# Optimization experiments

Measured on AMD Instinct MI355X. Metric: run time of the kernel, lower is better.

## Reference

```python
import jax, jax.numpy as jnp
import numpy as np

LOG_STD_MAX = 2.0
LOG_STD_MIN = -5.0
HEIGHT = 4          # tree height -> 16 leaves, 15 internal nodes
TOP_K = 4           # top-k leaves kept in soft gate
SMAX_TEMP = 1.0     # softmax temperature over selected leaf logits


def _path_matrix(height: int) -> np.ndarray:
    """[N_internal, L] matrix with +1 where a leaf's root-to-leaf path goes
    left through a node, -1 where it goes right, 0 otherwise."""
    L = 2 ** height
    P = np.zeros((L - 1, L), dtype=np.float32)
    for leaf in range(L):
        node = 0
        for lvl in range(height):
            bit = (leaf >> (height - 1 - lvl)) & 1
            P[node, leaf] = 1.0 if bit == 0 else -1.0
            node = 2 * node + 1 + bit
    return P


def setup_inputs() -> dict:
    key = jax.random.key(0)
    k0, k1, k2, k3, k4 = jax.random.split(key, 5)
    B, D, A = 262144, 128, 8
    L = 2 ** HEIGHT
    N = L - 1
    x = jax.random.normal(k0, (B, D), dtype=jnp.float32)
    Wn = jax.random.normal(k1, (D, N), dtype=jnp.float32) / np.float32(np.sqrt(D))
    bn = jax.random.normal(k2, (N,), dtype=jnp.float32) * 0.01
    Wl = jax.random.normal(k3, (L, D, 2 * A), dtype=jnp.float32) / np.float32(np.sqrt(D))
    bl = jax.random.normal(k4, (L, 2 * A), dtype=jnp.float32) * 0.01
    return {"x": x, "Wn": Wn, "bn": bn, "Wl": Wl, "bl": bl}


def reference(x, Wn, bn, Wl, bl):
    L = Wl.shape[0]
    P = jnp.asarray(_path_matrix(HEIGHT))              # [N, L] constant

    # --- differentiable-tree routing ---
    node_logits = x @ Wn + bn                          # [B, N]
    leaf_logits = node_logits @ P                      # [B, L]
    vals, idx = jax.lax.top_k(leaf_logits, TOP_K)      # [B, k]
    soft = jax.nn.softmax(vals / SMAX_TEMP, axis=-1)   # [B, k]
    onehot = jax.nn.one_hot(idx, L, dtype=x.dtype)     # [B, k, L]
    gate_soft = jnp.einsum('bk,bkl->bl', soft, onehot) # scatter soft weights
    gate_hard = onehot[:, 0]                           # argmax leaf one-hot
    # hard argmax forward, top-k softmax gradient (straight-through)
    gate = gate_hard + gate_soft - jax.lax.stop_gradient(gate_soft)

    # --- per-leaf linear controllers, gated sum ---
    leaf_out = jnp.einsum('bd,ldo->blo', x, Wl) + bl   # [B, L, 2A]
    out = jnp.einsum('bl,blo->bo', gate, leaf_out)     # [B, 2A]

    A = out.shape[-1] // 2
    mean, log_std = out[:, :A], out[:, A:]
    log_std = jnp.tanh(log_std)
    log_std = LOG_STD_MIN + 0.5 * (LOG_STD_MAX - LOG_STD_MIN) * (log_std + 1.0)
    return mean, log_std
```

## Files before the change

kernel.cpp:

```cpp
#include <hip/hip_runtime.h>
#include <math.h>

#define BLK  256
#define DD   128
#define NN   15
#define NL   16
#define OC   16
#define OSTR 20
#define MAXT 32
#define TPW  8
#define GAPTHR 1e-3f

typedef __attribute__((ext_vector_type(8))) short short8v;
typedef __attribute__((ext_vector_type(4))) float f32x4;
typedef union { unsigned u[4]; short8v s; } fragu;

__device__ inline unsigned bf16_rne_u(float f) {
    unsigned u = __float_as_uint(f);
    return (u + 0x7FFFu + ((u >> 16) & 1u)) >> 16;
}
__device__ inline unsigned cvt_pk_bf16(float a, float b) {
    unsigned r;
    asm volatile("v_cvt_pk_bf16_f32 %0, %1, %2" : "=v"(r) : "v"(a), "v"(b));
    return r;
}
__device__ inline void split8(const float v[8], short8v& hi, short8v& lo) {
    fragu H, L;
    #pragma unroll
    for (int p = 0; p < 4; ++p) {
        const float a = v[2*p], b = v[2*p+1];
        const unsigned h = cvt_pk_bf16(a, b);
        H.u[p] = h;
        const float ra = a - __uint_as_float(h << 16);
        const float rb = b - __uint_as_float(h & 0xFFFF0000u);
        L.u[p] = cvt_pk_bf16(ra, rb);
    }
    hi = H.s; lo = L.s;
}
__device__ inline short8v pack8hi(const float v[8]) {
    fragu H;
    #pragma unroll
    for (int p = 0; p < 4; ++p) H.u[p] = cvt_pk_bf16(v[2*p], v[2*p+1]);
    return H.s;
}

__global__ __launch_bounds__(256)
void dts_prep(const float* __restrict__ Wn, const float* __restrict__ Wl,
              unsigned short* __restrict__ wlB,
              unsigned short* __restrict__ wnHi, unsigned short* __restrict__ wnLo)
{
    const int id = blockIdx.x * 256 + threadIdx.x;
    if (id < 32768) {
        const int j = id & 7, n = (id >> 3) & 15, g = (id >> 7) & 3,
                  c = (id >> 9) & 3, leaf = id >> 11;
        const int k = c * 32 + g * 8 + j;
        wlB[id] = (unsigned short)bf16_rne_u(Wl[((size_t)leaf * DD + k) * OC + n]);
    } else if (id < 32768 + 2048) {
        const int id2 = id - 32768;
        const int j = id2 & 7, n = (id2 >> 3) & 15, g = (id2 >> 7) & 3, c = id2 >> 9;
        const int k = c * 32 + g * 8 + j;
        const float v = (n < NN) ? Wn[k * NN + n] : 0.f;
        const unsigned hb = bf16_rne_u(v);
        wnHi[id2] = (unsigned short)hb;
        wnLo[id2] = (unsigned short)bf16_rne_u(v - __uint_as_float(hb << 16));
    }
}

__global__ __launch_bounds__(BLK, 4)
void dts_fused10(const float* __restrict__ x, const float* __restrict__ Wn,
                 const float* __restrict__ bn, const float* __restrict__ bl,
                 const unsigned short* __restrict__ wlB,
                 const unsigned short* __restrict__ wnHi,
                 const unsigned short* __restrict__ wnLo,
                 float* __restrict__ out, int B)
{
    __shared__ __align__(16) float sXch[BLK * OSTR];
    __shared__ float sBn[NN];
    __shared__ __align__(16) float sBl[NL * OC];
    __shared__ int sPerm[BLK];
    __shared__ int sBins[NL];
    __shared__ int sStarts[NL];
    __shared__ int sTleaf[MAXT];
    __shared__ int sTm0[MAXT];
    __shared__ int sTend[MAXT];
    __shared__ int sNT;

    const int t    = threadIdx.x;
    const int wv   = t >> 6;
    const int lane = t & 63;
    const int lo16 = t & 15;
    const int grp  = (t >> 4) & 3;
    const int rowBase = blockIdx.x * BLK;

    if (t < NN) sBn[t] = bn[t];
    for (int i = t; i < NL * OC; i += BLK) sBl[i] = bl[i];
    if (t < NL) sBins[t] = 0;
    __syncthreads();

    const int waveRow0 = rowBase + wv * 64;
    f32x4 accn[4];
    #pragma unroll
    for (int i = 0; i < 4; ++i) accn[i] = (f32x4){0.f, 0.f, 0.f, 0.f};

    #pragma unroll 1
    for (int c = 0; c < 4; ++c) {
        const short8v bh = *(const short8v*)&wnHi[(c * 64 + lane) * 8];
        const short8v bw = *(const short8v*)&wnLo[(c * 64 + lane) * 8];
        #pragma unroll
        for (int i = 0; i < 4; ++i) {
            const float* ap = x + (size_t)(waveRow0 + i * 16 + lo16) * DD + c * 32 + grp * 8;
            const float4 a0 = *(const float4*)ap;
            const float4 a1 = *(const float4*)(ap + 4);
            float av[8];
            av[0]=a0.x; av[1]=a0.y; av[2]=a0.z; av[3]=a0.w;
            av[4]=a1.x; av[5]=a1.y; av[6]=a1.z; av[7]=a1.w;
            short8v ah, al;
            split8(av, ah, al);
            accn[i] = __builtin_amdgcn_mfma_f32_16x16x32_bf16(ah, bh, accn[i], 0, 0, 0);
            accn[i] = __builtin_amdgcn_mfma_f32_16x16x32_bf16(al, bh, accn[i], 0, 0, 0);
            accn[i] = __builtin_amdgcn_mfma_f32_16x16x32_bf16(ah, bw, accn[i], 0, 0, 0);
        }
    }

    {
        float* patch = &sXch[wv * 64 * OSTR];
        #pragma unroll
        for (int i = 0; i < 4; ++i)
            #pragma unroll
            for (int j = 0; j < 4; ++j)
                patch[(i * 16 + grp * 4 + j) * OSTR + lo16] = accn[i][j];
    }
    asm volatile("s_waitcnt lgkmcnt(0)" ::: "memory");
    __builtin_amdgcn_sched_barrier(0);

    float nl[16];
    {
        const float4* np = (const float4*)&sXch[t * OSTR];
        const float4 n0 = np[0], n1 = np[1], n2 = np[2], n3 = np[3];
        nl[0]=n0.x; nl[1]=n0.y; nl[2]=n0.z;  nl[3]=n0.w;
        nl[4]=n1.x; nl[5]=n1.y; nl[6]=n1.z;  nl[7]=n1.w;
        nl[8]=n2.x; nl[9]=n2.y; nl[10]=n2.z; nl[11]=n2.w;
        nl[12]=n3.x; nl[13]=n3.y; nl[14]=n3.z;
    }
    #pragma unroll
    for (int n = 0; n < NN; ++n) nl[n] += sBn[n];

    float L2a[4], L3a[8], L4a[16];
    #define EXPAND(src) { \
        float p = src[0], m = -src[0]; \
        L2a[0] = p + src[1]; L2a[1] = p - src[1]; \
        L2a[2] = m + src[2]; L2a[3] = m - src[2]; \
        _Pragma("unroll") \
        for (int i = 0; i < 4; ++i) { L3a[2*i] = L2a[i] + src[3+i]; L3a[2*i+1] = L2a[i] - src[3+i]; } \
        _Pragma("unroll") \
        for (int i = 0; i < 8; ++i) { L4a[2*i] = L3a[i] + src[7+i]; L4a[2*i+1] = L3a[i] - src[7+i]; } }
    EXPAND(nl)
    int best = 0; float bv = L4a[0], sv = -1e30f;
    #pragma unroll
    for (int l = 1; l < NL; ++l) {
        if (L4a[l] > bv) { sv = bv; bv = L4a[l]; best = l; }
        else if (L4a[l] > sv) sv = L4a[l];
    }

    if (bv - sv < GAPTHR) {
        float e[NN];
        #pragma unroll
        for (int n = 0; n < NN; ++n) e[n] = 0.f;
        const float* xrow = x + (size_t)(rowBase + t) * DD;
        for (int d = 0; d < DD; ++d) {
            const float xd = xrow[d];
            const float* wr = Wn + d * NN;
            #pragma unroll
            for (int n = 0; n < NN; ++n) e[n] = fmaf(xd, wr[n], e[n]);
        }
        #pragma unroll
        for (int n = 0; n < NN; ++n) e[n] += sBn[n];
        EXPAND(e)
        best = 0; bv = L4a[0];
        #pragma unroll
        for (int l = 1; l < NL; ++l) if (L4a[l] > bv) { bv = L4a[l]; best = l; }
    }
    #undef EXPAND

    const int rank = atomicAdd(&sBins[best], 1);
    __syncthreads();
    if (t == 0) {
        int s = 0, nt = 0;
        #pragma unroll
        for (int l = 0; l < NL; ++l) {
            sStarts[l] = s;
            const int cn = sBins[l];
            for (int m0 = s; m0 < s + cn; m0 += 16) {
                sTleaf[nt] = l; sTm0[nt] = m0; sTend[nt] = s + cn; ++nt;
            }
            s += cn;
        }
        sNT = nt;
    }
    __syncthreads();
    sPerm[sStarts[best] + rank] = t;
    __syncthreads();
    const int nT = sNT;

    int tleaf[TPW], tm0[TPW], tend[TPW], prow[TPW];
    #pragma unroll
    for (int i = 0; i < TPW; ++i) {
        const int tid = wv + i * 4;
        const bool vld = tid < nT;
        tleaf[i] = vld ? sTleaf[tid] : 0;
        tm0[i]   = vld ? sTm0[tid]   : 0;
        tend[i]  = vld ? sTend[tid]  : 0;
        prow[i]  = sPerm[tm0[i] + lo16];
    }
    f32x4 accm[TPW];
    #pragma unroll
    for (int i = 0; i < TPW; ++i) accm[i] = (f32x4){0.f, 0.f, 0.f, 0.f};

    #pragma unroll 1
    for (int c = 0; c < 4; ++c) {
        #pragma unroll
        for (int i = 0; i < TPW; ++i) {
            if (wv + i * 4 < nT) {
                const float* ap = x + (size_t)(rowBase + prow[i]) * DD + c * 32 + grp * 8;
                const float4 a0 = *(const float4*)ap;
                const float4 a1 = *(const float4*)(ap + 4);
                float av[8];
                av[0]=a0.x; av[1]=a0.y; av[2]=a0.z; av[3]=a0.w;
                av[4]=a1.x; av[5]=a1.y; av[6]=a1.z; av[7]=a1.w;
                const short8v ah = pack8hi(av);
                const short8v bf = *(const short8v*)&wlB[tleaf[i] * 2048 + (c * 64 + lane) * 8];
                accm[i] = __builtin_amdgcn_mfma_f32_16x16x32_bf16(ah, bf, accm[i], 0, 0, 0);
            }
        }
    }

    __syncthreads();
    #pragma unroll
    for (int i = 0; i < TPW; ++i) {
        if (wv + i * 4 < nT) {
            const float bias = sBl[tleaf[i] * OC + lo16];
            #pragma unroll
            for (int j = 0; j < 4; ++j) {
                const int sl = tm0[i] + grp * 4 + j;
                if (sl < tend[i]) sXch[sPerm[sl] * OSTR + lo16] = accm[i][j] + bias;
            }
        }
    }
    __syncthreads();
    {
        const float* so = &sXch[t * OSTR];
        const float4 m0 = *(const float4*)(so);
        const float4 m1 = *(const float4*)(so + 4);
        const float4 s0 = *(const float4*)(so + 8);
        const float4 s1 = *(const float4*)(so + 12);

        const size_t ob = (size_t)(rowBase + t) * 8;
        *reinterpret_cast<float4*>(&out[ob])     = m0;
        *reinterpret_cast<float4*>(&out[ob + 4]) = m1;

        float4 r0, r1;
        #define SQ(v) (-1.5f + 3.5f * (1.f - 2.f / (__expf(2.f * (v)) + 1.f)))
        r0.x = SQ(s0.x); r0.y = SQ(s0.y); r0.z = SQ(s0.z); r0.w = SQ(s0.w);
        r1.x = SQ(s1.x); r1.y = SQ(s1.y); r1.z = SQ(s1.z); r1.w = SQ(s1.w);
        #undef SQ
        const size_t ob2 = (size_t)B * 8 + ob;
        *reinterpret_cast<float4*>(&out[ob2])     = r0;
        *reinterpret_cast<float4*>(&out[ob2 + 4]) = r1;
    }
}

extern "C" void kernel_launch(void* const* d_in, const int* in_sizes, int n_in,
                              void* d_out, int out_size, void* d_ws, size_t ws_size,
                              hipStream_t stream)
{
    const float* x  = (const float*)d_in[0];
    const float* Wn = (const float*)d_in[1];
    const float* bn = (const float*)d_in[2];
    const float* Wl = (const float*)d_in[3];
    const float* bl = (const float*)d_in[4];
    float* out = (float*)d_out;

    unsigned short* wlB  = (unsigned short*)d_ws;
    unsigned short* wnHi = wlB + 32768;
    unsigned short* wnLo = wnHi + 2048;

    const int B = in_sizes[0] / DD;
    const int blocks = (B + BLK - 1) / BLK;

    hipLaunchKernelGGL(dts_prep, dim3(136), dim3(256), 0, stream, Wn, Wl, wlB, wnHi, wnLo);
    hipLaunchKernelGGL(dts_fused10, dim3(blocks), dim3(BLK), 0, stream,
                       x, Wn, bn, bl, wlB, wnHi, wnLo, out, B);
}
```

Before: 74.33 us.

## Compute all sixteen leaf controllers densely and select per row, dropping leaf sort

Replaces the per-block bucket sort of rows by argmax leaf (atomics, prefix scan, permutation, several barriers, and gathered reloads of x) with a dense pass. Each wave runs MFMAs for every one of the 16 leaves over its own 64 rows and keeps only the result for each row's selected leaf. The bf16 hi fragments of x from the routing GEMM are kept in registers and reused, so x is not re-read from global memory. This does 16x the leaf MFMA work and raises register pressure (occupancy hint lowered from 4 to 3) in exchange for removing synchronisation, divergence and the second x load.

```diff
diff --git a/kernel.cpp b/kernel.cpp
--- a/kernel.cpp
+++ b/kernel.cpp
@@ -7,8 +7,6 @@
 #define NL   16
 #define OC   16
 #define OSTR 20
-#define MAXT 32
-#define TPW  8
 #define GAPTHR 1e-3f
 
 typedef __attribute__((ext_vector_type(8))) short short8v;
@@ -36,12 +34,6 @@
         L.u[p] = cvt_pk_bf16(ra, rb);
     }
     hi = H.s; lo = L.s;
-}
-__device__ inline short8v pack8hi(const float v[8]) {
-    fragu H;
-    #pragma unroll
-    for (int p = 0; p < 4; ++p) H.u[p] = cvt_pk_bf16(v[2*p], v[2*p+1]);
-    return H.s;
 }
 
 __global__ __launch_bounds__(256)
@@ -66,8 +58,8 @@
     }
 }
 
-__global__ __launch_bounds__(BLK, 4)
-void dts_fused10(const float* __restrict__ x, const float* __restrict__ Wn,
+__global__ __launch_bounds__(BLK, 3)
+void dts_fused11(const float* __restrict__ x, const float* __restrict__ Wn,
                  const float* __restrict__ bn, const float* __restrict__ bl,
                  const unsigned short* __restrict__ wlB,
                  const unsigned short* __restrict__ wnHi,
@@ -77,13 +69,7 @@
     __shared__ __align__(16) float sXch[BLK * OSTR];
     __shared__ float sBn[NN];
     __shared__ __align__(16) float sBl[NL * OC];
-    __shared__ int sPerm[BLK];
-    __shared__ int sBins[NL];
-    __shared__ int sStarts[NL];
-    __shared__ int sTleaf[MAXT];
-    __shared__ int sTm0[MAXT];
-    __shared__ int sTend[MAXT];
-    __shared__ int sNT;
+    __shared__ unsigned char sLeaf[BLK];
 
     const int t    = threadIdx.x;
     const int wv   = t >> 6;
@@ -94,15 +80,15 @@
 
     if (t < NN) sBn[t] = bn[t];
     for (int i = t; i < NL * OC; i += BLK) sBl[i] = bl[i];
-    if (t < NL) sBins[t] = 0;
     __syncthreads();
 
     const int waveRow0 = rowBase + wv * 64;
+    short8v ah[4][4];
     f32x4 accn[4];
     #pragma unroll
     for (int i = 0; i < 4; ++i) accn[i] = (f32x4){0.f, 0.f, 0.f, 0.f};
 
-    #pragma unroll 1
+    #pragma unroll
     for (int c = 0; c < 4; ++c) {
         const short8v bh = *(const short8v*)&wnHi[(c * 64 + lane) * 8];
         const short8v bw = *(const short8v*)&wnLo[(c * 64 + lane) * 8];
@@ -114,12 +100,14 @@
             float av[8];
             av[0]=a0.x; av[1]=a0.y; av[2]=a0.z; av[3]=a0.w;
             av[4]=a1.x; av[5]=a1.y; av[6]=a1.z; av[7]=a1.w;
-            short8v ah, al;
-            split8(av, ah, al);
-            accn[i] = __builtin_amdgcn_mfma_f32_16x16x32_bf16(ah, bh, accn[i], 0, 0, 0);
-            accn[i] = __builtin_amdgcn_mfma_f32_16x16x32_bf16(al, bh, accn[i], 0, 0, 0);
-            accn[i] = __builtin_amdgcn_mfma_f32_16x16x32_bf16(ah, bw, accn[i], 0, 0, 0);
+            short8v hi, lo;
+            split8(av, hi, lo);
+            ah[c][i] = hi;
+            accn[i] = __builtin_amdgcn_mfma_f32_16x16x32_bf16(hi, bh, accn[i], 0, 0, 0);
+            accn[i] = __builtin_amdgcn_mfma_f32_16x16x32_bf16(lo, bh, accn[i], 0, 0, 0);
+            accn[i] = __builtin_amdgcn_mfma_f32_16x16x32_bf16(hi, bw, accn[i], 0, 0, 0);
         }
+        __builtin_amdgcn_sched_barrier(0);
     }
 
     {
@@ -182,71 +170,54 @@
     }
     #undef EXPAND
 
-    const int rank = atomicAdd(&sBins[best], 1);
-    __syncthreads();
-    if (t == 0) {
-        int s = 0, nt = 0;
-        #pragma unroll
-        for (int l = 0; l < NL; ++l) {
-            sStarts[l] = s;
-            const int cn = sBins[l];
-            for (int m0 = s; m0 < s + cn; m0 += 16) {
-                sTleaf[nt] = l; sTm0[nt] = m0; sTend[nt] = s + cn; ++nt;
+    sLeaf[t] = (unsigned char)best;
+    asm volatile("s_waitcnt lgkmcnt(0)" ::: "memory");
+    __builtin_amdgcn_sched_barrier(0);
+
+    unsigned lfp[4];
+    #pragma unroll
+    for (int rt = 0; rt < 4; ++rt)
+        lfp[rt] = *(const unsigned*)&sLeaf[wv * 64 + rt * 16 + grp * 4];
+
+    f32x4 keep[4];
+    #pragma unroll
+    for (int rt = 0; rt < 4; ++rt) keep[rt] = (f32x4){0.f, 0.f, 0.f, 0.f};
+
+    #pragma unroll 1
+    for (int nt = 0; nt < NL; ++nt) {
+        short8v bf[4];
+        #pragma unroll
+        for (int c = 0; c < 4; ++c)
+            bf[c] = *(const short8v*)&wlB[nt * 2048 + (c * 64 + lane) * 8];
+        f32x4 acc[4];
+        #pragma unroll
+        for (int rt = 0; rt < 4; ++rt) acc[rt] = (f32x4){0.f, 0.f, 0.f, 0.f};
+        #pragma unroll
+        for (int c = 0; c < 4; ++c)
+            #pragma unroll
+            for (int rt = 0; rt < 4; ++rt)
+                acc[rt] = __builtin_amdgcn_mfma_f32_16x16x32_bf16(ah[c][rt], bf[c], acc[rt], 0, 0, 0);
+        #pragma unroll
+        for (int rt = 0; rt < 4; ++rt)
+            #pragma unroll
+            for (int j = 0; j < 4; ++j)
+                keep[rt][j] = (((lfp[rt] >> (8 * j)) & 0xFFu) == (unsigned)nt)
+                            ? acc[rt][j] : keep[rt][j];
+    }
+
+    {
+        float* patch = &sXch[wv * 64 * OSTR];
+        #pragma unroll
+        for (int rt = 0; rt < 4; ++rt)
+            #pragma unroll
+            for (int j = 0; j < 4; ++j) {
+                const int lf = (lfp[rt] >> (8 * j)) & 0xFF;
+                patch[(rt * 16 + grp * 4 + j) * OSTR + lo16] =
+                    keep[rt][j] + sBl[lf * OC + lo16];
             }
-            s += cn;
-        }
-        sNT = nt;
-    }
-    __syncthreads();
-    sPerm[sStarts[best] + rank] = t;
-    __syncthreads();
-    const int nT = sNT;
-
-    int tleaf[TPW], tm0[TPW], tend[TPW], prow[TPW];
-    #pragma unroll
-    for (int i = 0; i < TPW; ++i) {
-        const int tid = wv + i * 4;
-        const bool vld = tid < nT;
-        tleaf[i] = vld ? sTleaf[tid] : 0;
-        tm0[i]   = vld ? sTm0[tid]   : 0;
-        tend[i]  = vld ? sTend[tid]  : 0;
-        prow[i]  = sPerm[tm0[i] + lo16];
-    }
-    f32x4 accm[TPW];
-    #pragma unroll
-    for (int i = 0; i < TPW; ++i) accm[i] = (f32x4){0.f, 0.f, 0.f, 0.f};
-
-    #pragma unroll 1
-    for (int c = 0; c < 4; ++c) {
-        #pragma unroll
-        for (int i = 0; i < TPW; ++i) {
-            if (wv + i * 4 < nT) {
-                const float* ap = x + (size_t)(rowBase + prow[i]) * DD + c * 32 + grp * 8;
-                const float4 a0 = *(const float4*)ap;
-                const float4 a1 = *(const float4*)(ap + 4);
-                float av[8];
-                av[0]=a0.x; av[1]=a0.y; av[2]=a0.z; av[3]=a0.w;
-                av[4]=a1.x; av[5]=a1.y; av[6]=a1.z; av[7]=a1.w;
-                const short8v ah = pack8hi(av);
-                const short8v bf = *(const short8v*)&wlB[tleaf[i] * 2048 + (c * 64 + lane) * 8];
-                accm[i] = __builtin_amdgcn_mfma_f32_16x16x32_bf16(ah, bf, accm[i], 0, 0, 0);
-            }
-        }
-    }
-
-    __syncthreads();
-    #pragma unroll
-    for (int i = 0; i < TPW; ++i) {
-        if (wv + i * 4 < nT) {
-            const float bias = sBl[tleaf[i] * OC + lo16];
-            #pragma unroll
-            for (int j = 0; j < 4; ++j) {
-                const int sl = tm0[i] + grp * 4 + j;
-                if (sl < tend[i]) sXch[sPerm[sl] * OSTR + lo16] = accm[i][j] + bias;
-            }
-        }
-    }
-    __syncthreads();
+    }
+    asm volatile("s_waitcnt lgkmcnt(0)" ::: "memory");
+    __builtin_amdgcn_sched_barrier(0);
     {
         const float* so = &sXch[t * OSTR];
         const float4 m0 = *(const float4*)(so);
@@ -288,6 +259,6 @@
     const int blocks = (B + BLK - 1) / BLK;
 
     hipLaunchKernelGGL(dts_prep, dim3(136), dim3(256), 0, stream, Wn, Wl, wlB, wnHi, wnLo);
-    hipLaunchKernelGGL(dts_fused10, dim3(blocks), dim3(BLK), 0, stream,
+    hipLaunchKernelGGL(dts_fused11, dim3(blocks), dim3(BLK), 0, stream,
                        x, Wn, bn, bl, wlB, wnHi, wnLo, out, B);
 }
```

Result: faster. 62.11 us (-16.4%).
